# Performance work log

Hardware: AMD Instinct MI355X
Metric: run time of the kernel (lower is better)

Reference implementation:

```python
import jax, jax.numpy as jnp
import numpy as np

THRESHOLD = 0.005
EPS = 1e-5  # torch instance_norm default eps


def setup_inputs() -> dict:
    key = jax.random.key(0)
    k1, k2, k3 = jax.random.split(key, 3)
    B, C, H, W = 4, 64, 64, 64
    feat = 64
    stdv = 1.0 / np.sqrt(feat)  # matches __init_W_bias__ uniform(-stdv, stdv)
    x = jax.random.normal(k1, (B, C, H, W), dtype=jnp.float32)
    W0 = jax.random.uniform(k2, (1, feat, feat), dtype=jnp.float32, minval=-stdv, maxval=stdv)
    W1 = jax.random.uniform(k3, (1, feat, feat), dtype=jnp.float32, minval=-stdv, maxval=stdv)
    return {"x": x, "W0": W0, "W1": W1}


def _laplacian(xn):
    # xn: [B, N, C] node features (pixels x channels). Built under no_grad in torch.
    norms = jnp.sqrt(jnp.sum(xn * xn, axis=2, keepdims=True))  # [B, N, 1]
    num = jnp.einsum('bnc,bmc->bnm', xn, xn)                    # [B, N, N]
    corr = num / (norms * jnp.swapaxes(norms, 1, 2))
    # relu then threshold -> binary adjacency (threshold > 0, so relu is subsumed)
    A = (corr > THRESHOLD).astype(xn.dtype)
    deg = jnp.sum(A, axis=2)                                    # [B, N]
    d_is = 1.0 / jnp.sqrt(deg)                                  # inverse(sqrt(D)) is diagonal
    return A * d_is[:, :, None] * d_is[:, None, :]              # D^-1/2 A D^-1/2


def _instance_norm(h):
    # torch F.instance_norm on [B, N, F] normalizes over the last dim per (b, n)
    mean = jnp.mean(h, axis=-1, keepdims=True)
    var = jnp.mean((h - mean) ** 2, axis=-1, keepdims=True)
    return (h - mean) / jnp.sqrt(var + EPS)


def reference(x, W0, W1):
    B, C, H, Wd = x.shape
    x_linear = x.reshape(B, C, H * Wd).transpose(0, 2, 1)  # [B, N, C]
    lap = _laplacian(jax.lax.stop_gradient(x_linear))       # adjacency built with no_grad
    for Wk in (W0, W1):
        lx = jnp.einsum('bnm,bmc->bnc', lap, x_linear)      # laplacian diffusion
        h = jnp.einsum('bnc,cf->bnf', lx, Wk[0])            # shared weight (repeat over batch)
        x_linear = jax.nn.relu(_instance_norm(h))
    return x_linear
```

## Files before the change

kernel.cpp:

```cpp
#include <hip/hip_runtime.h>
#include <hip/hip_bf16.h>
#include <cstdint>

#define BB 4
#define CC 64
#define NN 4096
#define NWRD 64
#define TAU 0.005f
#define EPSN 1e-5f
#define MSPLITS 8

typedef __attribute__((ext_vector_type(8))) short short8;
typedef __attribute__((ext_vector_type(4))) float f32x4;
typedef unsigned long long ull;

__device__ inline unsigned int bf16_rne(float v) {
    unsigned int u = __float_as_uint(v);
    return (u + 0x7FFFu + ((u >> 16) & 1u)) >> 16;
}

__global__ __launch_bounds__(256) void k_transpose(const float* __restrict__ x,
                                                   float* __restrict__ xt,
                                                   unsigned short* __restrict__ ynh,
                                                   unsigned short* __restrict__ ynl,
                                                   int* __restrict__ deg) {
    __shared__ float lds[64 * 65];
    int t = threadIdx.x;
    int b = blockIdx.y;
    int n0 = blockIdx.x * 64;
    int gid = (b * (NN / 64) + blockIdx.x) * 256 + t;
    if (gid < BB * NN) deg[gid] = 0;
    #pragma unroll
    for (int i = 0; i < 4; ++i) {
        int c = i * 16 + (t >> 4);
        int nc = (t & 15) * 4;
        float4 v = *(const float4*)(x + ((size_t)(b * CC + c)) * NN + n0 + nc);
        lds[c * 65 + nc + 0] = v.x;
        lds[c * 65 + nc + 1] = v.y;
        lds[c * 65 + nc + 2] = v.z;
        lds[c * 65 + nc + 3] = v.w;
    }
    __syncthreads();
    int l = t & 63, wv = t >> 6;
    for (int i = 0; i < 16; ++i) {
        int n = wv * 16 + i;
        float v = lds[l * 65 + n];
        float s = v * v;
        #pragma unroll
        for (int off = 32; off; off >>= 1) s += __shfl_xor(s, off, 64);
        float yv = v * rsqrtf(s);
        unsigned int hb = bf16_rne(yv);
        float lo = yv - __uint_as_float(hb << 16);
        unsigned int lb = bf16_rne(lo);
        size_t row = (size_t)(b * NN + n0 + n);
        xt[row * CC + l] = v;
        ynh[row * CC + l] = (unsigned short)hb;
        ynl[row * CC + l] = (unsigned short)lb;
    }
}

#define CORR_MC 128
__global__ __launch_bounds__(256) void k_corr(const unsigned short* __restrict__ ynh,
                                              const unsigned short* __restrict__ ynl,
                                              ull* __restrict__ mask,
                                              int* __restrict__ deg) {
    __shared__ unsigned short ldsH[CORR_MC * 64];
    __shared__ unsigned short ldsL[CORR_MC * 64];
    int t = threadIdx.x;
    int l = t & 63, wv = t >> 6;
    int lc = l & 15, q = l >> 4;
    int b = blockIdx.z;
    int n0 = blockIdx.x * 256 + wv * 64;
    int m0 = blockIdx.y * 512;
    const unsigned short* bH = ynh + (size_t)b * NN * CC;
    const unsigned short* bL = ynl + (size_t)b * NN * CC;

    short8 ah[4][2], al[4][2];
    #pragma unroll
    for (int nt = 0; nt < 4; ++nt)
        #pragma unroll
        for (int ks = 0; ks < 2; ++ks) {
            size_t off = (size_t)(n0 + nt * 16 + lc) * CC + (ks * 4 + q) * 8;
            ah[nt][ks] = *(const short8*)(bH + off);
            al[nt][ks] = *(const short8*)(bL + off);
        }

    int rr = l & 15;
    int rsel = rr & 3;
    int qq = rr >> 2;
    int myq = l >> 4;

    for (int mc = 0; mc < 4; ++mc) {
        __syncthreads();
        int mbase = m0 + mc * CORR_MC;
        #pragma unroll
        for (int rd = 0; rd < 4; ++rd) {
            int g = rd * 256 + t;
            int row = g >> 3, c = g & 7;
            uint4 vh = *(const uint4*)(bH + (size_t)(mbase + row) * CC + c * 8);
            uint4 vl = *(const uint4*)(bL + (size_t)(mbase + row) * CC + c * 8);
            int sw = (c ^ (row & 7)) * 8;
            *(uint4*)&ldsH[row * 64 + sw] = vh;
            *(uint4*)&ldsL[row * 64 + sw] = vl;
        }
        __syncthreads();
        ull w0 = 0, w1 = 0;
        #pragma unroll
        for (int tt = 0; tt < 8; ++tt) {
            short8 bh[2], bl[2];
            #pragma unroll
            for (int ks = 0; ks < 2; ++ks) {
                int rowm = tt * 16 + lc;
                int sw = ((ks * 4 + q) ^ (rowm & 7)) * 8;
                bh[ks] = *(const short8*)&ldsH[rowm * 64 + sw];
                bl[ks] = *(const short8*)&ldsL[rowm * 64 + sw];
            }
            #pragma unroll
            for (int nt = 0; nt < 4; ++nt) {
                f32x4 acc = {0.f, 0.f, 0.f, 0.f};
                #pragma unroll
                for (int ks = 0; ks < 2; ++ks) {
                    acc = __builtin_amdgcn_mfma_f32_16x16x32_bf16(ah[nt][ks], bh[ks], acc, 0, 0, 0);
                    acc = __builtin_amdgcn_mfma_f32_16x16x32_bf16(ah[nt][ks], bl[ks], acc, 0, 0, 0);
                    acc = __builtin_amdgcn_mfma_f32_16x16x32_bf16(al[nt][ks], bh[ks], acc, 0, 0, 0);
                }
                ull bal[4];
                #pragma unroll
                for (int r = 0; r < 4; ++r)
                    bal[r] = __ballot(acc[r] > TAU);
                ull sa = (rsel & 1) ? bal[1] : bal[0];
                ull sb = (rsel & 1) ? bal[3] : bal[2];
                ull sel = (rsel & 2) ? sb : sa;
                ull part = ((sel >> (qq * 16)) & 0xFFFFull) << ((tt & 3) * 16);
                if (myq == nt) { if (tt < 4) w0 |= part; else w1 |= part; }
            }
        }
        int row = n0 + myq * 16 + rr;
        int wbase = (mbase >> 6);
        mask[((size_t)(b * NN + row)) * NWRD + wbase + 0] = w0;
        mask[((size_t)(b * NN + row)) * NWRD + wbase + 1] = w1;
        atomicAdd(&deg[b * NN + row], __popcll(w0) + __popcll(w1));
    }
}

__global__ __launch_bounds__(256) void k_pack(const float* __restrict__ xin,
                                              const int* __restrict__ deg,
                                              unsigned short* __restrict__ yph) {
    __shared__ float lds[32 * 65];
    int t = threadIdx.x;
    int kt = blockIdx.x;
    int b = blockIdx.y;
    size_t ibase = (size_t)b * NN * CC + (size_t)kt * 32 * CC;
    #pragma unroll
    for (int i = 0; i < 2; ++i) {
        int f4 = i * 256 + t;
        int m = f4 >> 4;
        float d = rsqrtf((float)deg[b * NN + kt * 32 + m]);
        float4 v = ((const float4*)(xin + ibase))[f4];
        int c = (f4 & 15) * 4;
        lds[m * 65 + c + 0] = v.x * d;
        lds[m * 65 + c + 1] = v.y * d;
        lds[m * 65 + c + 2] = v.z * d;
        lds[m * 65 + c + 3] = v.w * d;
    }
    __syncthreads();
    size_t obase = (size_t)b * NN * CC + (size_t)kt * 2048;
    int kin = t & 31;
    int chi = t >> 5;
    #pragma unroll
    for (int cg = 0; cg < 8; ++cg) {
        int c = cg * 8 + chi;
        yph[obase + c * 32 + kin] = (unsigned short)bf16_rne(lds[kin * 65 + c]);
    }
}

#define GMC 128
__global__ __launch_bounds__(256) void k_gemm(const ull* __restrict__ mask,
                                              const unsigned short* __restrict__ yph,
                                              float* __restrict__ plx) {
    __shared__ unsigned short ldsB[4 * 2048];
    int t = threadIdx.x;
    int l = t & 63, wv = t >> 6;
    int lc = l & 15, q = l >> 4;
    int b = blockIdx.z;
    int ms = blockIdx.y;
    int n0 = blockIdx.x * 256 + wv * 64;
    int m0 = ms * 512;
    const unsigned short* src = yph + (size_t)b * NN * CC;
    const ull* mrow[4];
    #pragma unroll
    for (int nt = 0; nt < 4; ++nt)
        mrow[nt] = mask + ((size_t)(b * NN + n0 + nt * 16 + lc)) * NWRD;

    f32x4 acc[4][4];
    #pragma unroll
    for (int nt = 0; nt < 4; ++nt)
        #pragma unroll
        for (int tt = 0; tt < 4; ++tt) acc[nt][tt] = f32x4{0.f, 0.f, 0.f, 0.f};

    for (int mc = 0; mc < 4; ++mc) {
        __syncthreads();
        int mbase = m0 + mc * GMC;
        int ktbase = mbase >> 5;
        #pragma unroll
        for (int rd = 0; rd < 4; ++rd) {
            int g = rd * 256 + t;
            uint4 v = *(const uint4*)(src + (size_t)ktbase * 2048 + g * 8);
            *(uint4*)&ldsB[g * 8] = v;
        }
        __syncthreads();
        int wbase = mbase >> 6;
        ull mw[4][2];
        #pragma unroll
        for (int nt = 0; nt < 4; ++nt) {
            mw[nt][0] = mrow[nt][wbase];
            mw[nt][1] = mrow[nt][wbase + 1];
        }
        #pragma unroll
        for (int kt = 0; kt < 4; ++kt) {
            int sh = (kt & 1) * 32 + q * 8;
            union { unsigned int u[4]; short8 v; } a[4];
            #pragma unroll
            for (int nt = 0; nt < 4; ++nt) {
                unsigned int bits = (unsigned int)(mw[nt][kt >> 1] >> sh) & 0xFFu;
                #pragma unroll
                for (int j = 0; j < 4; ++j)
                    a[nt].u[j] = ((bits >> (2 * j)) & 1u ? 0x3F80u : 0u)
                               | ((bits >> (2 * j + 1)) & 1u ? 0x3F800000u : 0u);
            }
            #pragma unroll
            for (int tt = 0; tt < 4; ++tt) {
                short8 bf = *(const short8*)&ldsB[kt * 2048 + (tt * 16 + lc) * 32 + q * 8];
                #pragma unroll
                for (int nt = 0; nt < 4; ++nt)
                    acc[nt][tt] = __builtin_amdgcn_mfma_f32_16x16x32_bf16(a[nt].v, bf, acc[nt][tt], 0, 0, 0);
            }
        }
    }
    #pragma unroll
    for (int nt = 0; nt < 4; ++nt)
        #pragma unroll
        for (int tt = 0; tt < 4; ++tt)
            #pragma unroll
            for (int r = 0; r < 4; ++r) {
                int n = n0 + nt * 16 + q * 4 + r;
                int c = tt * 16 + lc;
                plx[((size_t)((ms * BB + b)) * NN + n) * CC + c] = acc[nt][tt][r];
            }
}

__global__ __launch_bounds__(256) void k_out(const float* __restrict__ plx,
                                             const int* __restrict__ deg,
                                             const float* __restrict__ W,
                                             float* __restrict__ xout,
                                             unsigned short* __restrict__ xpack) {
    __shared__ float lxs[4][68];
    int lane = threadIdx.x & 63;
    int wave = threadIdx.x >> 6;
    int b = blockIdx.y;
    int n0 = blockIdx.x * 16 + wave * 4;
    float Wreg[64];
    #pragma unroll
    for (int c = 0; c < 64; ++c) Wreg[c] = W[c * 64 + lane];
    for (int tI = 0; tI < 4; ++tI) {
        int n = n0 + tI;
        size_t row = (size_t)(b * NN + n);
        float dRow = rsqrtf((float)deg[row]);
        float lx = 0.f;
        #pragma unroll
        for (int s = 0; s < MSPLITS; ++s)
            lx += plx[((size_t)(s * BB + b) * NN + n) * CC + lane];
        lx *= dRow;
        lxs[wave][lane] = lx;
        float h = 0.f;
        #pragma unroll
        for (int c4 = 0; c4 < 16; ++c4) {
            float4 s4 = *(const float4*)&lxs[wave][c4 * 4];
            h += s4.x * Wreg[c4 * 4 + 0] + s4.y * Wreg[c4 * 4 + 1]
               + s4.z * Wreg[c4 * 4 + 2] + s4.w * Wreg[c4 * 4 + 3];
        }
        float mean = h;
        #pragma unroll
        for (int off = 32; off; off >>= 1) mean += __shfl_xor(mean, off, 64);
        mean *= (1.f / 64.f);
        float dv = h - mean;
        float var = dv * dv;
        #pragma unroll
        for (int off = 32; off; off >>= 1) var += __shfl_xor(var, off, 64);
        var *= (1.f / 64.f);
        float o = dv * rsqrtf(var + EPSN);
        o = o > 0.f ? o : 0.f;
        if (xout)
            xout[row * CC + lane] = o;
        if (xpack)
            xpack[(size_t)b * NN * CC + (size_t)(n >> 5) * 2048 + lane * 32 + (n & 31)] =
                (unsigned short)bf16_rne(o * dRow);
    }
}

extern "C" void kernel_launch(void* const* d_in, const int* in_sizes, int n_in,
                              void* d_out, int out_size, void* d_ws, size_t ws_size,
                              hipStream_t stream) {
    const float* x  = (const float*)d_in[0];
    const float* W0 = (const float*)d_in[1];
    const float* W1 = (const float*)d_in[2];
    float* out = (float*)d_out;

    char* ws = (char*)d_ws;
    ull* mask = (ull*)(ws);
    float* xt = (float*)(ws + ((size_t)8 << 20));
    unsigned short* ynh = (unsigned short*)(ws + ((size_t)12 << 20));
    unsigned short* ynl = (unsigned short*)(ws + ((size_t)14 << 20));
    unsigned short* xp0 = (unsigned short*)(ws + ((size_t)16 << 20));
    unsigned short* xp1 = (unsigned short*)(ws + ((size_t)18 << 20));
    float* plx = (float*)(ws + ((size_t)20 << 20));
    int* deg = (int*)(ws + ((size_t)52 << 20));

    k_transpose<<<dim3(NN / 64, BB), 256, 0, stream>>>(x, xt, ynh, ynl, deg);
    k_corr<<<dim3(NN / 256, NN / 512, BB), 256, 0, stream>>>(ynh, ynl, mask, deg);

    k_pack<<<dim3(128, BB), 256, 0, stream>>>(xt, deg, xp0);
    k_gemm<<<dim3(NN / 256, MSPLITS, BB), 256, 0, stream>>>(mask, xp0, plx);
    k_out<<<dim3(NN / 16, BB), 256, 0, stream>>>(plx, deg, W0, nullptr, xp1);

    k_gemm<<<dim3(NN / 256, MSPLITS, BB), 256, 0, stream>>>(mask, xp1, plx);
    k_out<<<dim3(NN / 16, BB), 256, 0, stream>>>(plx, deg, W1, out, nullptr);
}
```

Baseline: 155.7 us.

## Drop LDS staging in mask GEMM and halve per-wave row tile

The mask-times-features GEMM no longer stages B tiles through shared memory with block barriers. Each wave now loads its bf16 B fragments straight from global memory into registers, and the per-wave row tile shrinks from 64 to 32 rows, which doubles the grid. This removes the __syncthreads and LDS traffic and adds parallelism. In exchange, B data is reused less across the row tiles in a block, so global and L2 reads of the packed features go up, and the 16 short8 fragments raise register pressure.

```diff
diff --git a/kernel.cpp b/kernel.cpp
--- a/kernel.cpp
+++ b/kernel.cpp
@@ -174,71 +174,62 @@
     }
 }
 
-#define GMC 128
 __global__ __launch_bounds__(256) void k_gemm(const ull* __restrict__ mask,
                                               const unsigned short* __restrict__ yph,
                                               float* __restrict__ plx) {
-    __shared__ unsigned short ldsB[4 * 2048];
     int t = threadIdx.x;
     int l = t & 63, wv = t >> 6;
     int lc = l & 15, q = l >> 4;
     int b = blockIdx.z;
     int ms = blockIdx.y;
-    int n0 = blockIdx.x * 256 + wv * 64;
+    int n0 = blockIdx.x * 128 + wv * 32;
     int m0 = ms * 512;
     const unsigned short* src = yph + (size_t)b * NN * CC;
-    const ull* mrow[4];
-    #pragma unroll
-    for (int nt = 0; nt < 4; ++nt)
-        mrow[nt] = mask + ((size_t)(b * NN + n0 + nt * 16 + lc)) * NWRD;
-
-    f32x4 acc[4][4];
-    #pragma unroll
-    for (int nt = 0; nt < 4; ++nt)
+    const ull* mrow0 = mask + ((size_t)(b * NN + n0 + lc)) * NWRD;
+    const ull* mrow1 = mask + ((size_t)(b * NN + n0 + 16 + lc)) * NWRD;
+
+    f32x4 acc[2][4];
+    #pragma unroll
+    for (int nt = 0; nt < 2; ++nt)
         #pragma unroll
         for (int tt = 0; tt < 4; ++tt) acc[nt][tt] = f32x4{0.f, 0.f, 0.f, 0.f};
 
+    #pragma unroll
     for (int mc = 0; mc < 4; ++mc) {
-        __syncthreads();
-        int mbase = m0 + mc * GMC;
+        int mbase = m0 + mc * 128;
         int ktbase = mbase >> 5;
-        #pragma unroll
-        for (int rd = 0; rd < 4; ++rd) {
-            int g = rd * 256 + t;
-            uint4 v = *(const uint4*)(src + (size_t)ktbase * 2048 + g * 8);
-            *(uint4*)&ldsB[g * 8] = v;
-        }
-        __syncthreads();
         int wbase = mbase >> 6;
-        ull mw[4][2];
-        #pragma unroll
-        for (int nt = 0; nt < 4; ++nt) {
-            mw[nt][0] = mrow[nt][wbase];
-            mw[nt][1] = mrow[nt][wbase + 1];
-        }
+        ull mw0a = mrow0[wbase], mw0b = mrow0[wbase + 1];
+        ull mw1a = mrow1[wbase], mw1b = mrow1[wbase + 1];
+        short8 bf[4][4];
+        #pragma unroll
+        for (int kt = 0; kt < 4; ++kt)
+            #pragma unroll
+            for (int tt = 0; tt < 4; ++tt)
+                bf[kt][tt] = *(const short8*)(src + (size_t)(ktbase + kt) * 2048
+                                              + (tt * 16 + lc) * 32 + q * 8);
         #pragma unroll
         for (int kt = 0; kt < 4; ++kt) {
             int sh = (kt & 1) * 32 + q * 8;
-            union { unsigned int u[4]; short8 v; } a[4];
-            #pragma unroll
-            for (int nt = 0; nt < 4; ++nt) {
-                unsigned int bits = (unsigned int)(mw[nt][kt >> 1] >> sh) & 0xFFu;
-                #pragma unroll
-                for (int j = 0; j < 4; ++j)
-                    a[nt].u[j] = ((bits >> (2 * j)) & 1u ? 0x3F80u : 0u)
-                               | ((bits >> (2 * j + 1)) & 1u ? 0x3F800000u : 0u);
+            unsigned int bits0 = (unsigned int)(((kt < 2) ? mw0a : mw0b) >> sh) & 0xFFu;
+            unsigned int bits1 = (unsigned int)(((kt < 2) ? mw1a : mw1b) >> sh) & 0xFFu;
+            union { unsigned int u[4]; short8 v; } a0, a1;
+            #pragma unroll
+            for (int j = 0; j < 4; ++j) {
+                a0.u[j] = ((bits0 >> (2 * j)) & 1u ? 0x3F80u : 0u)
+                        | ((bits0 >> (2 * j + 1)) & 1u ? 0x3F800000u : 0u);
+                a1.u[j] = ((bits1 >> (2 * j)) & 1u ? 0x3F80u : 0u)
+                        | ((bits1 >> (2 * j + 1)) & 1u ? 0x3F800000u : 0u);
             }
             #pragma unroll
             for (int tt = 0; tt < 4; ++tt) {
-                short8 bf = *(const short8*)&ldsB[kt * 2048 + (tt * 16 + lc) * 32 + q * 8];
-                #pragma unroll
-                for (int nt = 0; nt < 4; ++nt)
-                    acc[nt][tt] = __builtin_amdgcn_mfma_f32_16x16x32_bf16(a[nt].v, bf, acc[nt][tt], 0, 0, 0);
-            }
-        }
-    }
-    #pragma unroll
-    for (int nt = 0; nt < 4; ++nt)
+                acc[0][tt] = __builtin_amdgcn_mfma_f32_16x16x32_bf16(a0.v, bf[kt][tt], acc[0][tt], 0, 0, 0);
+                acc[1][tt] = __builtin_amdgcn_mfma_f32_16x16x32_bf16(a1.v, bf[kt][tt], acc[1][tt], 0, 0, 0);
+            }
+        }
+    }
+    #pragma unroll
+    for (int nt = 0; nt < 2; ++nt)
         #pragma unroll
         for (int tt = 0; tt < 4; ++tt)
             #pragma unroll
@@ -320,9 +311,9 @@
     k_corr<<<dim3(NN / 256, NN / 512, BB), 256, 0, stream>>>(ynh, ynl, mask, deg);
 
     k_pack<<<dim3(128, BB), 256, 0, stream>>>(xt, deg, xp0);
-    k_gemm<<<dim3(NN / 256, MSPLITS, BB), 256, 0, stream>>>(mask, xp0, plx);
+    k_gemm<<<dim3(NN / 128, MSPLITS, BB), 256, 0, stream>>>(mask, xp0, plx);
     k_out<<<dim3(NN / 16, BB), 256, 0, stream>>>(plx, deg, W0, nullptr, xp1);
 
-    k_gemm<<<dim3(NN / 256, MSPLITS, BB), 256, 0, stream>>>(mask, xp1, plx);
+    k_gemm<<<dim3(NN / 128, MSPLITS, BB), 256, 0, stream>>>(mask, xp1, plx);
     k_out<<<dim3(NN / 16, BB), 256, 0, stream>>>(plx, deg, W1, out, nullptr);
 }
```

Measured after the change: 174.4 us. 12.0% more time.

## Double-buffer LDS tiles with async global-to-LDS loads in corr and gemm kernels

Applied to the files above, without the earlier changes.

Both the correlation and the masked-GEMM kernels now stage their B tiles through two LDS buffers, filled with direct global_load_lds DMA. The next tile is prefetched while MFMAs run on the current one, and one barrier per iteration is removed. The correlation kernel moves the XOR swizzle onto the global source address so the LDS writes can stay linear. The GEMM kernel also loads all of its adjacency-mask words into registers up front. In exchange, LDS use doubles and register pressure rises, and correctness depends on the compiler waiting for the outstanding LDS-DMA loads before each barrier.

```diff
diff --git a/kernel.cpp b/kernel.cpp
--- a/kernel.cpp
+++ b/kernel.cpp
@@ -17,6 +17,12 @@
 __device__ inline unsigned int bf16_rne(float v) {
     unsigned int u = __float_as_uint(v);
     return (u + 0x7FFFu + ((u >> 16) & 1u)) >> 16;
+}
+
+__device__ inline void gload_lds16(const void* g, void* lds_base) {
+    __builtin_amdgcn_global_load_lds(
+        (const __attribute__((address_space(1))) unsigned int*)g,
+        (__attribute__((address_space(3))) unsigned int*)lds_base, 16, 0, 0);
 }
 
 __global__ __launch_bounds__(256) void k_transpose(const float* __restrict__ x,
@@ -64,8 +70,8 @@
                                               const unsigned short* __restrict__ ynl,
                                               ull* __restrict__ mask,
                                               int* __restrict__ deg) {
-    __shared__ unsigned short ldsH[CORR_MC * 64];
-    __shared__ unsigned short ldsL[CORR_MC * 64];
+    __shared__ unsigned short ldsH[2][CORR_MC * 64];
+    __shared__ unsigned short ldsL[2][CORR_MC * 64];
     int t = threadIdx.x;
     int l = t & 63, wv = t >> 6;
     int lc = l & 15, q = l >> 4;
@@ -90,20 +96,24 @@
     int qq = rr >> 2;
     int myq = l >> 4;
 
+    auto stage = [&](int mc, int bufi) {
+        int mbase = m0 + mc * CORR_MC;
+        #pragma unroll
+        for (int rd = 0; rd < 4; ++rd) {
+            int gu = rd * 256 + wv * 64;
+            int g = gu + l;
+            int ci = (g & ~7) | ((g & 7) ^ ((g >> 3) & 7));
+            gload_lds16(bH + (size_t)mbase * CC + ci * 8, &ldsH[bufi][gu * 8]);
+            gload_lds16(bL + (size_t)mbase * CC + ci * 8, &ldsL[bufi][gu * 8]);
+        }
+    };
+
+    stage(0, 0);
     for (int mc = 0; mc < 4; ++mc) {
         __syncthreads();
+        if (mc + 1 < 4) stage(mc + 1, (mc + 1) & 1);
+        int bufi = mc & 1;
         int mbase = m0 + mc * CORR_MC;
-        #pragma unroll
-        for (int rd = 0; rd < 4; ++rd) {
-            int g = rd * 256 + t;
-            int row = g >> 3, c = g & 7;
-            uint4 vh = *(const uint4*)(bH + (size_t)(mbase + row) * CC + c * 8);
-            uint4 vl = *(const uint4*)(bL + (size_t)(mbase + row) * CC + c * 8);
-            int sw = (c ^ (row & 7)) * 8;
-            *(uint4*)&ldsH[row * 64 + sw] = vh;
-            *(uint4*)&ldsL[row * 64 + sw] = vl;
-        }
-        __syncthreads();
         ull w0 = 0, w1 = 0;
         #pragma unroll
         for (int tt = 0; tt < 8; ++tt) {
@@ -112,8 +122,8 @@
             for (int ks = 0; ks < 2; ++ks) {
                 int rowm = tt * 16 + lc;
                 int sw = ((ks * 4 + q) ^ (rowm & 7)) * 8;
-                bh[ks] = *(const short8*)&ldsH[rowm * 64 + sw];
-                bl[ks] = *(const short8*)&ldsL[rowm * 64 + sw];
+                bh[ks] = *(const short8*)&ldsH[bufi][rowm * 64 + sw];
+                bl[ks] = *(const short8*)&ldsL[bufi][rowm * 64 + sw];
             }
             #pragma unroll
             for (int nt = 0; nt < 4; ++nt) {
@@ -178,7 +188,7 @@
 __global__ __launch_bounds__(256) void k_gemm(const ull* __restrict__ mask,
                                               const unsigned short* __restrict__ yph,
                                               float* __restrict__ plx) {
-    __shared__ unsigned short ldsB[4 * 2048];
+    __shared__ unsigned short ldsB[2][4 * 2048];
     int t = threadIdx.x;
     int l = t & 63, wv = t >> 6;
     int lc = l & 15, q = l >> 4;
@@ -187,42 +197,45 @@
     int n0 = blockIdx.x * 256 + wv * 64;
     int m0 = ms * 512;
     const unsigned short* src = yph + (size_t)b * NN * CC;
-    const ull* mrow[4];
+
+    ull mw[4][4][2];
+    #pragma unroll
+    for (int nt = 0; nt < 4; ++nt) {
+        const ull* mrow = mask + ((size_t)(b * NN + n0 + nt * 16 + lc)) * NWRD + (m0 >> 6);
+        #pragma unroll
+        for (int mc = 0; mc < 4; ++mc) {
+            mw[mc][nt][0] = mrow[mc * 2];
+            mw[mc][nt][1] = mrow[mc * 2 + 1];
+        }
+    }
+
+    f32x4 acc[4][4];
     #pragma unroll
     for (int nt = 0; nt < 4; ++nt)
-        mrow[nt] = mask + ((size_t)(b * NN + n0 + nt * 16 + lc)) * NWRD;
-
-    f32x4 acc[4][4];
-    #pragma unroll
-    for (int nt = 0; nt < 4; ++nt)
         #pragma unroll
         for (int tt = 0; tt < 4; ++tt) acc[nt][tt] = f32x4{0.f, 0.f, 0.f, 0.f};
 
+    auto stage = [&](int mc, int bufi) {
+        int ktbase = (m0 + mc * GMC) >> 5;
+        #pragma unroll
+        for (int rd = 0; rd < 4; ++rd) {
+            int gu = rd * 256 + wv * 64;
+            gload_lds16(src + (size_t)ktbase * 2048 + (gu + l) * 8, &ldsB[bufi][gu * 8]);
+        }
+    };
+
+    stage(0, 0);
     for (int mc = 0; mc < 4; ++mc) {
         __syncthreads();
-        int mbase = m0 + mc * GMC;
-        int ktbase = mbase >> 5;
-        #pragma unroll
-        for (int rd = 0; rd < 4; ++rd) {
-            int g = rd * 256 + t;
-            uint4 v = *(const uint4*)(src + (size_t)ktbase * 2048 + g * 8);
-            *(uint4*)&ldsB[g * 8] = v;
-        }
-        __syncthreads();
-        int wbase = mbase >> 6;
-        ull mw[4][2];
-        #pragma unroll
-        for (int nt = 0; nt < 4; ++nt) {
-            mw[nt][0] = mrow[nt][wbase];
-            mw[nt][1] = mrow[nt][wbase + 1];
-        }
+        if (mc + 1 < 4) stage(mc + 1, (mc + 1) & 1);
+        int bufi = mc & 1;
         #pragma unroll
         for (int kt = 0; kt < 4; ++kt) {
             int sh = (kt & 1) * 32 + q * 8;
             union { unsigned int u[4]; short8 v; } a[4];
             #pragma unroll
             for (int nt = 0; nt < 4; ++nt) {
-                unsigned int bits = (unsigned int)(mw[nt][kt >> 1] >> sh) & 0xFFu;
+                unsigned int bits = (unsigned int)(mw[mc][nt][kt >> 1] >> sh) & 0xFFu;
                 #pragma unroll
                 for (int j = 0; j < 4; ++j)
                     a[nt].u[j] = ((bits >> (2 * j)) & 1u ? 0x3F80u : 0u)
@@ -230,7 +243,7 @@
             }
             #pragma unroll
             for (int tt = 0; tt < 4; ++tt) {
-                short8 bf = *(const short8*)&ldsB[kt * 2048 + (tt * 16 + lc) * 32 + q * 8];
+                short8 bf = *(const short8*)&ldsB[bufi][kt * 2048 + (tt * 16 + lc) * 32 + q * 8];
                 #pragma unroll
                 for (int nt = 0; nt < 4; ++nt)
                     acc[nt][tt] = __builtin_amdgcn_mfma_f32_16x16x32_bf16(a[nt].v, bf, acc[nt][tt], 0, 0, 0);
```

After: 154.1 us. About the same (-1.0%).
